# Kernel optimization log

Hardware: AMD Instinct MI355X
Metric: run time of the kernel (lower is better)

Reference implementation:

```python
import jax, jax.numpy as jnp
import numpy as np

D_MODEL = 1024
N_HEADS = 16
D_K = D_MODEL // N_HEADS


def setup_inputs() -> dict:
    key = jax.random.key(0)
    ks = jax.random.split(key, 12)
    B, S, D, H = 2, 2048, D_MODEL, N_HEADS
    s = 1.0 / np.sqrt(D)
    inp = {
        "x": jax.random.normal(ks[0], (B, S, D), jnp.float32),
        "Wq": jax.random.normal(ks[1], (D, D), jnp.float32) * s,
        "bq": jnp.zeros((D,), jnp.float32),
        "Wk": jax.random.normal(ks[2], (D, D), jnp.float32) * s,
        "bk": jnp.zeros((D,), jnp.float32),
        "Wv": jax.random.normal(ks[3], (D, D), jnp.float32) * s,
        "bv": jnp.zeros((D,), jnp.float32),
        "Wo": jax.random.normal(ks[4], (D, D), jnp.float32) * s,
        "bo": jnp.zeros((D,), jnp.float32),
        "Wp": jax.random.normal(ks[5], (D, H), jnp.float32) * s,
        "bp": jnp.zeros((H,), jnp.float32),
        "alpha": jax.random.normal(ks[6], (H,), jnp.float32) * 0.1,
    }
    return inp


def reference(x, Wq, bq, Wk, bk, Wv, bv, Wo, bo, Wp, bp, alpha):
    B, S, D = x.shape
    H, dk = N_HEADS, D_K
    scale = dk ** -0.5
    # projections -> (B, H, S, dk)
    Q = (x @ Wq + bq).reshape(B, S, H, dk).transpose(0, 2, 1, 3)
    K = (x @ Wk + bk).reshape(B, S, H, dk).transpose(0, 2, 1, 3)
    V = (x @ Wv + bv).reshape(B, S, H, dk).transpose(0, 2, 1, 3)
    scores = jnp.einsum("bhid,bhjd->bhij", Q, K) * scale  # (B,H,S,S)
    # phase derived from x: (B,S,H) -> (B,H,S)
    phase = (x @ Wp + bp).transpose(0, 2, 1)
    # coherence(i,j) = cos(phi_i - phi_j), per batch/head
    coherence = jnp.cos(phase[:, :, :, None] - phase[:, :, None, :])
    scores = scores + alpha[None, :, None, None] * coherence
    attn = jax.nn.softmax(scores, axis=-1)
    out = jnp.einsum("bhij,bhjd->bhid", attn, V)  # (B,H,S,dk)
    out = out.transpose(0, 2, 1, 3).reshape(B, S, D)
    return out @ Wo + bo
```

## Files before the change

kernel.cpp:

```cpp
#include <hip/hip_runtime.h>
#include <math.h>


#define S_LEN 2048
#define NHEADS 16

typedef __attribute__((ext_vector_type(8))) short short8;
typedef __attribute__((ext_vector_type(4))) float floatx4;
typedef __attribute__((ext_vector_type(2))) float float2v;

__device__ inline unsigned short f2bf(float f) {
    union { float f; unsigned int i; } v; v.f = f;
    unsigned int u = v.i;
    return (unsigned short)((u + 0x7fffu + ((u >> 16) & 1u)) >> 16);
}
__device__ inline unsigned int pack2_bf16(float hi, float lo) {
    union { float f; unsigned int u; } a, b; a.f = hi; b.f = lo;
    return __builtin_amdgcn_perm(a.u, b.u, 0x07060302u);
}
__device__ inline void async_copy16(const unsigned short* src, unsigned short* dst_lds) {
    __builtin_amdgcn_global_load_lds(
        (const __attribute__((address_space(1))) unsigned int*)(src),
        (__attribute__((address_space(3))) unsigned int*)(dst_lds), 16, 0, 0);
}
__device__ inline void async_copy4(const float* src, float* dst_lds) {
    __builtin_amdgcn_global_load_lds(
        (const __attribute__((address_space(1))) unsigned int*)(src),
        (__attribute__((address_space(3))) unsigned int*)(dst_lds), 4, 0, 0);
}

__global__ __launch_bounds__(256) void prep_kernel(
    const float* __restrict__ x, const float* __restrict__ Wp,
    const float* __restrict__ bp,
    const float* __restrict__ w0, const float* __restrict__ w1,
    const float* __restrict__ w2, const float* __restrict__ w3,
    unsigned short* __restrict__ d0, unsigned short* __restrict__ d1,
    unsigned short* __restrict__ d2, unsigned short* __restrict__ d3,
    float* __restrict__ cosP, float* __restrict__ sinP,
    unsigned short* __restrict__ xb) {
    __shared__ __align__(16) unsigned short shmem[64 * 72];
    int t = threadIdx.x;
    if (blockIdx.x < 4096) {
        float* fb = reinterpret_cast<float*>(shmem);
        float* xs = fb;
        float4* red4 = reinterpret_cast<float4*>(fb + 1024);
        int bid = blockIdx.x;
        int b = bid >> 11, s = bid & 2047;
        const float* xr = x + (size_t)bid * 1024;
        float4 xv = *reinterpret_cast<const float4*>(&xr[t * 4]);
        {
            uint2 o;
            o.x = (unsigned int)f2bf(xv.x) | ((unsigned int)f2bf(xv.y) << 16);
            o.y = (unsigned int)f2bf(xv.z) | ((unsigned int)f2bf(xv.w) << 16);
            *reinterpret_cast<uint2*>(&xb[(size_t)bid * 1024 + t * 4]) = o;
        }
        *reinterpret_cast<float4*>(&xs[t * 4]) = xv;
        __syncthreads();
        float f0 = 0.f, f1 = 0.f, f2 = 0.f, f3 = 0.f;
        int krow = t >> 2;
        const float4* wp4 = reinterpret_cast<const float4*>(Wp);
#pragma unroll
        for (int i = 0; i < 16; i++) {
            float4 wv = wp4[i * 256 + t];
            float xk = xs[i * 64 + krow];
            f0 += xk * wv.x; f1 += xk * wv.y; f2 += xk * wv.z; f3 += xk * wv.w;
        }
        red4[t] = make_float4(f0, f1, f2, f3);
        __syncthreads();
        if (t < 16) {
            int b2 = t >> 2, comp = t & 3;
            const float* rf = fb + 1024;
            float sum = bp[t];
#pragma unroll
            for (int j = 0; j < 64; j++) sum += rf[(4 * j + b2) * 4 + comp];
            float sv, cv;
            __sincosf(sum, &sv, &cv);
            size_t o = ((size_t)b * NHEADS + t) * S_LEN + s;
            cosP[o] = cv; sinP[o] = sv;
        }
    } else {
        unsigned short (*tile)[72] = reinterpret_cast<unsigned short (*)[72]>(shmem);
        int bid = blockIdx.x - 4096;
        int mat = bid >> 8;
        int tl  = bid & 255;
        int tr = tl >> 4, tc = tl & 15;
        const float* src    = (mat == 0) ? w0 : (mat == 1) ? w1 : (mat == 2) ? w2 : w3;
        unsigned short* dst = (mat == 0) ? d0 : (mat == 1) ? d1 : (mat == 2) ? d2 : d3;
        int col = t & 63, rbase = (t >> 6) * 16;
#pragma unroll
        for (int i = 0; i < 16; i++) {
            int row = rbase + i;
            tile[row][col] = f2bf(src[(size_t)(tr * 64 + row) * 1024 + tc * 64 + col]);
        }
        __syncthreads();
#pragma unroll
        for (int i = 0; i < 16; i++) {
            int row = rbase + i;
            dst[(size_t)(tc * 64 + row) * 1024 + tr * 64 + col] = tile[col][row];
        }
    }
}

template <int MT>
__global__ __launch_bounds__(256) void gemm_bt(
    const unsigned short* __restrict__ A, const unsigned short* __restrict__ BT,
    int N, int mode,
    const float* __restrict__ b0, const float* __restrict__ b1,
    const float* __restrict__ b2,
    unsigned short* __restrict__ o0, unsigned short* __restrict__ o1,
    unsigned short* __restrict__ o2, float* __restrict__ of) {
    __shared__ __align__(16) unsigned short As[2][MT * 32];
    __shared__ __align__(16) unsigned short Bs[2][128 * 32];
    const int K = 1024;
    const int MI = MT / 32;
    int t = threadIdx.x;
    int mBase = blockIdx.x * MT;
    int nBase = blockIdx.y * 128;
    int w = t >> 6, lane = t & 63, l15 = lane & 15, quad = lane >> 4;
    int wm = (w & 1) * (MT / 2), wn = (w >> 1) * 64;
    floatx4 acc[MI][4];
#pragma unroll
    for (int i = 0; i < MI; i++)
#pragma unroll
        for (int j = 0; j < 4; j++) acc[i][j] = (floatx4){0.f, 0.f, 0.f, 0.f};

    int arow = t >> 2, aseg = (t & 3) * 8;
#pragma unroll
    for (int i = 0; i < MT / 64; i++)
        async_copy16(&A[(size_t)(mBase + i * 64 + arow) * K + aseg],
                     &As[0][(i * 64 + arow) * 32 + aseg]);
#pragma unroll
    for (int i = 0; i < 2; i++)
        async_copy16(&BT[(size_t)(nBase + i * 64 + arow) * K + aseg],
                     &Bs[0][(i * 64 + arow) * 32 + aseg]);

    for (int k0 = 0; k0 < K; k0 += 32) {
        int cur = (k0 >> 5) & 1;
        __syncthreads();
        if (k0 + 32 < K) {
            int nb = cur ^ 1, kn = k0 + 32;
#pragma unroll
            for (int i = 0; i < MT / 64; i++)
                async_copy16(&A[(size_t)(mBase + i * 64 + arow) * K + kn + aseg],
                             &As[nb][(i * 64 + arow) * 32 + aseg]);
#pragma unroll
            for (int i = 0; i < 2; i++)
                async_copy16(&BT[(size_t)(nBase + i * 64 + arow) * K + kn + aseg],
                             &Bs[nb][(i * 64 + arow) * 32 + aseg]);
        }
        short8 af[MI], bfr[4];
#pragma unroll
        for (int mi = 0; mi < MI; mi++)
            af[mi] = *reinterpret_cast<const short8*>(&As[cur][(wm + mi * 16 + l15) * 32 + quad * 8]);
#pragma unroll
        for (int ni = 0; ni < 4; ni++)
            bfr[ni] = *reinterpret_cast<const short8*>(&Bs[cur][(wn + ni * 16 + l15) * 32 + quad * 8]);
        __builtin_amdgcn_s_setprio(1);
#pragma unroll
        for (int mi = 0; mi < MI; mi++)
#pragma unroll
            for (int ni = 0; ni < 4; ni++)
                acc[mi][ni] = __builtin_amdgcn_mfma_f32_16x16x32_bf16(af[mi], bfr[ni], acc[mi][ni], 0, 0, 0);
        __builtin_amdgcn_s_setprio(0);
    }

#pragma unroll
    for (int mi = 0; mi < MI; mi++) {
        int rowB = mBase + wm + mi * 16 + quad * 4;
#pragma unroll
        for (int ni = 0; ni < 4; ni++) {
            int col = nBase + wn + ni * 16 + l15;
            if (mode == 0) {
                float bias = b0[col];
#pragma unroll
                for (int r = 0; r < 4; r++) {
                    of[(size_t)(rowB + r) * N + col] = acc[mi][ni][r] + bias;
                }
            } else {
                int mat = col >> 10, nn = col & 1023;
                int h = nn >> 6, d = nn & 63;
                int b = rowB >> 11, sidx = rowB & 2047;
                if (mat == 2) {
                    float bv = b2[nn];
                    int jj = sidx & 63;
                    size_t rowOff = ((size_t)((b * NHEADS + h) * 64 + d)) * S_LEN +
                                    (sidx & ~63);
#pragma unroll
                    for (int r = 0; r < 4; r++) {
                        int j2 = jj + r;
                        int jt = j2 >> 4;
                        int u = (jt >> 1) * 32 + ((j2 & 15) >> 2) * 8 + (jt & 1) * 4 + (j2 & 3);
                        o2[rowOff + u] = f2bf(acc[mi][ni][r] + bv);
                    }
                } else {
                    const float* bias  = (mat == 0) ? b0 : b1;
                    unsigned short* op = (mat == 0) ? o0 : o1;
                    float bv = bias[nn];
                    float scl = (mat == 0) ? 0.18033688f : 1.0f;
#pragma unroll
                    for (int r = 0; r < 4; r++) {
                        float cv = (acc[mi][ni][r] + bv) * scl;
                        op[(((size_t)b * NHEADS + h) * S_LEN + (sidx + r)) * 64 + d] = f2bf(cv);
                    }
                }
            }
        }
    }
}

__global__ __launch_bounds__(1024) void attn_kernel(
    const unsigned short* __restrict__ Qg, const unsigned short* __restrict__ Kg,
    const unsigned short* __restrict__ VTg,
    const float* __restrict__ cosP, const float* __restrict__ sinP,
    const float* __restrict__ alpha, unsigned short* __restrict__ ctx) {
    __shared__ __align__(16) unsigned short KsB[4][64 * 64];
    __shared__ __align__(16) unsigned short VtB[4][64 * 64];
    __shared__ __align__(16) float csB[4][128];

    int x = blockIdx.x;
    int bh = (x & 7) * 4 + (x >> 6);
    int qt = (x >> 3) & 7;
    int t = threadIdx.x, w = t >> 6, lane = t & 63, l15 = lane & 15, quad = lane >> 4;
    int m0 = qt * 256 + w * 16;
    size_t base = (size_t)bh * (S_LEN * 64);
    size_t phBase = (size_t)bh * S_LEN;
    const float L2E = 1.44269504f;

    int th = t & 511;
    int sj = th >> 3, sg = th & 7;
    int srot = ((sg - (sj & 7)) & 7) * 8;
    bool stK = (t < 512);

    short8 qf[2];
#pragma unroll
    for (int c = 0; c < 2; c++)
        qf[c] = *reinterpret_cast<const short8*>(
            &Qg[base + (size_t)(m0 + l15) * 64 + c * 32 + quad * 8]);

    float alph = alpha[bh & 15] * L2E;
    float ci = alph * cosP[phBase + m0 + l15];
    float si = alph * sinP[phBase + m0 + l15];
    float2v ci2 = (float2v){ci, ci}, si2 = (float2v){si, si};

    {
#pragma unroll
        for (int t0 = 0; t0 < 2; t0++) {
            if (stK) async_copy16(&Kg[base + (size_t)(t0 * 64 + sj) * 64 + srot], &KsB[t0][th * 8]);
            else     async_copy16(&VTg[base + (size_t)sj * S_LEN + t0 * 64 + srot], &VtB[t0][th * 8]);
            if (w == 4)      async_copy4(&cosP[phBase + t0 * 64 + lane], &csB[t0][lane]);
            else if (w == 5) async_copy4(&sinP[phBase + t0 * 64 + lane], &csB[t0][64 + lane]);
        }
    }

    floatx4 oacc[4], lacc;
#pragma unroll
    for (int tt = 0; tt < 4; tt++) oacc[tt] = (floatx4){0.f, 0.f, 0.f, 0.f};
    lacc = (floatx4){0.f, 0.f, 0.f, 0.f};
    const short8 ones8 = {(short)0x3F80, (short)0x3F80, (short)0x3F80, (short)0x3F80,
                          (short)0x3F80, (short)0x3F80, (short)0x3F80, (short)0x3F80};

    int rot = l15 & 7;
    int cb0 = 16 * ((quad + rot) & 7);
    int cb1 = 16 * ((quad + 4 + rot) & 7);

    for (int kt = 0; kt < 32; kt++) {
        int p = kt & 3;
        if ((kt & 1) == 0) {
            __syncthreads();
#pragma unroll
            for (int d = 2; d <= 3; d++) {
                int kn = kt + d;
                if (kn < 32) {
                    int pn = kn & 3;
                    if (stK) async_copy16(&Kg[base + (size_t)(kn * 64 + sj) * 64 + srot], &KsB[pn][th * 8]);
                    else     async_copy16(&VTg[base + (size_t)sj * S_LEN + kn * 64 + srot], &VtB[pn][th * 8]);
                    if (w == 4)      async_copy4(&cosP[phBase + kn * 64 + lane], &csB[pn][lane]);
                    else if (w == 5) async_copy4(&sinP[phBase + kn * 64 + lane], &csB[pn][64 + lane]);
                }
            }
        }

        floatx4 st[4];
        __builtin_amdgcn_s_setprio(1);
#pragma unroll
        for (int jt = 0; jt < 4; jt++) {
            const char* kr = (const char*)&KsB[p][(jt * 16 + l15) * 64];
            short8 kf0 = *reinterpret_cast<const short8*>(kr + cb0);
            short8 kf1 = *reinterpret_cast<const short8*>(kr + cb1);
            floatx4 s = (floatx4){0.f, 0.f, 0.f, 0.f};
            s = __builtin_amdgcn_mfma_f32_16x16x32_bf16(kf0, qf[0], s, 0, 0, 0);
            s = __builtin_amdgcn_mfma_f32_16x16x32_bf16(kf1, qf[1], s, 0, 0, 0);
            st[jt] = s;
        }
        __builtin_amdgcn_s_setprio(0);

        union PW { unsigned int u[4]; short8 s8; };
        PW P0, P1;
#pragma unroll
        for (int jt = 0; jt < 4; jt++) {
            float4 cj4 = *reinterpret_cast<const float4*>(&csB[p][jt * 16 + quad * 4]);
            float4 sj4 = *reinterpret_cast<const float4*>(&csB[p][64 + jt * 16 + quad * 4]);
            float2v st01 = (float2v){st[jt][0], st[jt][1]};
            float2v st23 = (float2v){st[jt][2], st[jt][3]};
            float2v c01 = (float2v){cj4.x, cj4.y}, c23 = (float2v){cj4.z, cj4.w};
            float2v s01 = (float2v){sj4.x, sj4.y}, s23 = (float2v){sj4.z, sj4.w};
            float2v a01 = si2 * s01 + (ci2 * c01 + st01);
            float2v a23 = si2 * s23 + (ci2 * c23 + st23);
            unsigned int wA = pack2_bf16(__builtin_amdgcn_exp2f(a01.y),
                                         __builtin_amdgcn_exp2f(a01.x));
            unsigned int wB = pack2_bf16(__builtin_amdgcn_exp2f(a23.y),
                                         __builtin_amdgcn_exp2f(a23.x));
            if (jt == 0)      { P0.u[0] = wA; P0.u[1] = wB; }
            else if (jt == 1) { P0.u[2] = wA; P0.u[3] = wB; }
            else if (jt == 2) { P1.u[0] = wA; P1.u[1] = wB; }
            else              { P1.u[2] = wA; P1.u[3] = wB; }
        }

        __builtin_amdgcn_s_setprio(1);
#pragma unroll
        for (int c = 0; c < 2; c++) {
            short8 pf = c ? P1.s8 : P0.s8;
            int cb = c ? cb1 : cb0;
#pragma unroll
            for (int tt = 0; tt < 4; tt++) {
                const char* vr = (const char*)&VtB[p][(tt * 16 + l15) * 64];
                short8 vf = *reinterpret_cast<const short8*>(vr + cb);
                oacc[tt] = __builtin_amdgcn_mfma_f32_16x16x32_bf16(pf, vf, oacc[tt], 0, 0, 0);
            }
            lacc = __builtin_amdgcn_mfma_f32_16x16x32_bf16(pf, ones8, lacc, 0, 0, 0);
        }
        __builtin_amdgcn_s_setprio(0);
    }

    int b = bh >> 4, h = bh & 15;
    float inv[4];
#pragma unroll
    for (int r = 0; r < 4; r++) inv[r] = 1.0f / lacc[r];
#pragma unroll
    for (int tt = 0; tt < 4; tt++)
#pragma unroll
        for (int r = 0; r < 4; r++) {
            int srow = m0 + quad * 4 + r;
            ctx[((size_t)(b * S_LEN + srow)) * 1024 + h * 64 + tt * 16 + l15] =
                f2bf(oacc[tt][r] * inv[r]);
        }
}

extern "C" void kernel_launch(void* const* d_in, const int* in_sizes, int n_in,
                              void* d_out, int out_size, void* d_ws, size_t ws_size,
                              hipStream_t stream) {
    const float* x     = (const float*)d_in[0];
    const float* Wq    = (const float*)d_in[1];
    const float* bq    = (const float*)d_in[2];
    const float* Wk    = (const float*)d_in[3];
    const float* bk    = (const float*)d_in[4];
    const float* Wv    = (const float*)d_in[5];
    const float* bv    = (const float*)d_in[6];
    const float* Wo    = (const float*)d_in[7];
    const float* bo    = (const float*)d_in[8];
    const float* Wp    = (const float*)d_in[9];
    const float* bp    = (const float*)d_in[10];
    const float* alpha = (const float*)d_in[11];
    float* out = (float*)d_out;

    const size_t MB = 1048576;
    char* ws = (char*)d_ws;
    unsigned short* WT   = (unsigned short*)(ws);
    unsigned short* WoT  = (unsigned short*)(ws + 6 * MB);
    unsigned short* xb   = (unsigned short*)(ws + 8 * MB);
    unsigned short* ctx  = (unsigned short*)(ws + 8 * MB);
    unsigned short* Qw   = (unsigned short*)(ws + 16 * MB);
    unsigned short* Kw   = (unsigned short*)(ws + 24 * MB);
    unsigned short* VTg  = (unsigned short*)(ws + 32 * MB);
    float* cosP          = (float*)(ws + 40 * MB);
    float* sinP          = (float*)(ws + 40 * MB + 262144);

    prep_kernel<<<dim3(5120), dim3(256), 0, stream>>>(
        x, Wp, bp, Wq, Wk, Wv, Wo,
        WT, WT + 1048576, WT + 2097152, WoT, cosP, sinP, xb);
    gemm_bt<128><<<dim3(32, 24), dim3(256), 0, stream>>>(
        xb, WT, 3072, 1, bq, bk, bv, Qw, Kw, VTg, (float*)nullptr);
    attn_kernel<<<dim3(256), dim3(1024), 0, stream>>>(
        Qw, Kw, VTg, cosP, sinP, alpha, ctx);
    gemm_bt<64><<<dim3(64, 8), dim3(256), 0, stream>>>(
        ctx, WoT, 1024, 0, bo, bo, bo,
        (unsigned short*)nullptr, (unsigned short*)nullptr,
        (unsigned short*)nullptr, out);
}
```

Measured before the change: 203.5 us.

## Process 32 query rows per wave in attention to reuse K/V fragments

The attention kernel now runs 8 waves of 512 threads instead of 16 waves, and each wave handles two 16-row query sub-tiles. Each K and V fragment read from LDS, and each cos/sin value, now feeds two MFMAs, which halves LDS traffic per unit of work. Every thread now issues both the K and the V async copy. The cost is higher register pressure from doubled accumulators and fewer waves per CU to hide latency.

```diff
diff --git a/kernel.cpp b/kernel.cpp
--- a/kernel.cpp
+++ b/kernel.cpp
@@ -208,7 +208,7 @@
     }
 }
 
-__global__ __launch_bounds__(1024) void attn_kernel(
+__global__ __launch_bounds__(512) void attn_kernel(
     const unsigned short* __restrict__ Qg, const unsigned short* __restrict__ Kg,
     const unsigned short* __restrict__ VTg,
     const float* __restrict__ cosP, const float* __restrict__ sinP,
@@ -221,41 +221,48 @@
     int bh = (x & 7) * 4 + (x >> 6);
     int qt = (x >> 3) & 7;
     int t = threadIdx.x, w = t >> 6, lane = t & 63, l15 = lane & 15, quad = lane >> 4;
-    int m0 = qt * 256 + w * 16;
+    int m0 = qt * 256 + w * 32;
     size_t base = (size_t)bh * (S_LEN * 64);
     size_t phBase = (size_t)bh * S_LEN;
     const float L2E = 1.44269504f;
 
-    int th = t & 511;
-    int sj = th >> 3, sg = th & 7;
+    int sj = t >> 3, sg = t & 7;
     int srot = ((sg - (sj & 7)) & 7) * 8;
-    bool stK = (t < 512);
-
-    short8 qf[2];
-#pragma unroll
-    for (int c = 0; c < 2; c++)
-        qf[c] = *reinterpret_cast<const short8*>(
-            &Qg[base + (size_t)(m0 + l15) * 64 + c * 32 + quad * 8]);
+
+    short8 qf[2][2];
+#pragma unroll
+    for (int rh = 0; rh < 2; rh++)
+#pragma unroll
+        for (int c = 0; c < 2; c++)
+            qf[rh][c] = *reinterpret_cast<const short8*>(
+                &Qg[base + (size_t)(m0 + rh * 16 + l15) * 64 + c * 32 + quad * 8]);
 
     float alph = alpha[bh & 15] * L2E;
-    float ci = alph * cosP[phBase + m0 + l15];
-    float si = alph * sinP[phBase + m0 + l15];
-    float2v ci2 = (float2v){ci, ci}, si2 = (float2v){si, si};
+    float2v ci2[2], si2[2];
+#pragma unroll
+    for (int rh = 0; rh < 2; rh++) {
+        float ci = alph * cosP[phBase + m0 + rh * 16 + l15];
+        float si = alph * sinP[phBase + m0 + rh * 16 + l15];
+        ci2[rh] = (float2v){ci, ci}; si2[rh] = (float2v){si, si};
+    }
 
     {
 #pragma unroll
         for (int t0 = 0; t0 < 2; t0++) {
-            if (stK) async_copy16(&Kg[base + (size_t)(t0 * 64 + sj) * 64 + srot], &KsB[t0][th * 8]);
-            else     async_copy16(&VTg[base + (size_t)sj * S_LEN + t0 * 64 + srot], &VtB[t0][th * 8]);
+            async_copy16(&Kg[base + (size_t)(t0 * 64 + sj) * 64 + srot], &KsB[t0][t * 8]);
+            async_copy16(&VTg[base + (size_t)sj * S_LEN + t0 * 64 + srot], &VtB[t0][t * 8]);
             if (w == 4)      async_copy4(&cosP[phBase + t0 * 64 + lane], &csB[t0][lane]);
             else if (w == 5) async_copy4(&sinP[phBase + t0 * 64 + lane], &csB[t0][64 + lane]);
         }
     }
 
-    floatx4 oacc[4], lacc;
-#pragma unroll
-    for (int tt = 0; tt < 4; tt++) oacc[tt] = (floatx4){0.f, 0.f, 0.f, 0.f};
-    lacc = (floatx4){0.f, 0.f, 0.f, 0.f};
+    floatx4 oacc[2][4], lacc[2];
+#pragma unroll
+    for (int rh = 0; rh < 2; rh++) {
+#pragma unroll
+        for (int tt = 0; tt < 4; tt++) oacc[rh][tt] = (floatx4){0.f, 0.f, 0.f, 0.f};
+        lacc[rh] = (floatx4){0.f, 0.f, 0.f, 0.f};
+    }
     const short8 ones8 = {(short)0x3F80, (short)0x3F80, (short)0x3F80, (short)0x3F80,
                           (short)0x3F80, (short)0x3F80, (short)0x3F80, (short)0x3F80};
 
@@ -272,78 +279,97 @@
                 int kn = kt + d;
                 if (kn < 32) {
                     int pn = kn & 3;
-                    if (stK) async_copy16(&Kg[base + (size_t)(kn * 64 + sj) * 64 + srot], &KsB[pn][th * 8]);
-                    else     async_copy16(&VTg[base + (size_t)sj * S_LEN + kn * 64 + srot], &VtB[pn][th * 8]);
+                    async_copy16(&Kg[base + (size_t)(kn * 64 + sj) * 64 + srot], &KsB[pn][t * 8]);
+                    async_copy16(&VTg[base + (size_t)sj * S_LEN + kn * 64 + srot], &VtB[pn][t * 8]);
                     if (w == 4)      async_copy4(&cosP[phBase + kn * 64 + lane], &csB[pn][lane]);
                     else if (w == 5) async_copy4(&sinP[phBase + kn * 64 + lane], &csB[pn][64 + lane]);
                 }
             }
         }
 
-        floatx4 st[4];
+        floatx4 st[2][4];
         __builtin_amdgcn_s_setprio(1);
 #pragma unroll
         for (int jt = 0; jt < 4; jt++) {
             const char* kr = (const char*)&KsB[p][(jt * 16 + l15) * 64];
             short8 kf0 = *reinterpret_cast<const short8*>(kr + cb0);
             short8 kf1 = *reinterpret_cast<const short8*>(kr + cb1);
-            floatx4 s = (floatx4){0.f, 0.f, 0.f, 0.f};
-            s = __builtin_amdgcn_mfma_f32_16x16x32_bf16(kf0, qf[0], s, 0, 0, 0);
-            s = __builtin_amdgcn_mfma_f32_16x16x32_bf16(kf1, qf[1], s, 0, 0, 0);
-            st[jt] = s;
+#pragma unroll
+            for (int rh = 0; rh < 2; rh++) {
+                floatx4 s = (floatx4){0.f, 0.f, 0.f, 0.f};
+                s = __builtin_amdgcn_mfma_f32_16x16x32_bf16(kf0, qf[rh][0], s, 0, 0, 0);
+                s = __builtin_amdgcn_mfma_f32_16x16x32_bf16(kf1, qf[rh][1], s, 0, 0, 0);
+                st[rh][jt] = s;
+            }
         }
         __builtin_amdgcn_s_setprio(0);
 
+        float4 cj4[4], sj4[4];
+#pragma unroll
+        for (int jt = 0; jt < 4; jt++) {
+            cj4[jt] = *reinterpret_cast<const float4*>(&csB[p][jt * 16 + quad * 4]);
+            sj4[jt] = *reinterpret_cast<const float4*>(&csB[p][64 + jt * 16 + quad * 4]);
+        }
+
         union PW { unsigned int u[4]; short8 s8; };
-        PW P0, P1;
-#pragma unroll
-        for (int jt = 0; jt < 4; jt++) {
-            float4 cj4 = *reinterpret_cast<const float4*>(&csB[p][jt * 16 + quad * 4]);
-            float4 sj4 = *reinterpret_cast<const float4*>(&csB[p][64 + jt * 16 + quad * 4]);
-            float2v st01 = (float2v){st[jt][0], st[jt][1]};
-            float2v st23 = (float2v){st[jt][2], st[jt][3]};
-            float2v c01 = (float2v){cj4.x, cj4.y}, c23 = (float2v){cj4.z, cj4.w};
-            float2v s01 = (float2v){sj4.x, sj4.y}, s23 = (float2v){sj4.z, sj4.w};
-            float2v a01 = si2 * s01 + (ci2 * c01 + st01);
-            float2v a23 = si2 * s23 + (ci2 * c23 + st23);
-            unsigned int wA = pack2_bf16(__builtin_amdgcn_exp2f(a01.y),
-                                         __builtin_amdgcn_exp2f(a01.x));
-            unsigned int wB = pack2_bf16(__builtin_amdgcn_exp2f(a23.y),
-                                         __builtin_amdgcn_exp2f(a23.x));
-            if (jt == 0)      { P0.u[0] = wA; P0.u[1] = wB; }
-            else if (jt == 1) { P0.u[2] = wA; P0.u[3] = wB; }
-            else if (jt == 2) { P1.u[0] = wA; P1.u[1] = wB; }
-            else              { P1.u[2] = wA; P1.u[3] = wB; }
+        PW P0[2], P1[2];
+#pragma unroll
+        for (int rh = 0; rh < 2; rh++) {
+#pragma unroll
+            for (int jt = 0; jt < 4; jt++) {
+                float2v st01 = (float2v){st[rh][jt][0], st[rh][jt][1]};
+                float2v st23 = (float2v){st[rh][jt][2], st[rh][jt][3]};
+                float2v c01 = (float2v){cj4[jt].x, cj4[jt].y};
+                float2v c23 = (float2v){cj4[jt].z, cj4[jt].w};
+                float2v s01 = (float2v){sj4[jt].x, sj4[jt].y};
+                float2v s23 = (float2v){sj4[jt].z, sj4[jt].w};
+                float2v a01 = si2[rh] * s01 + (ci2[rh] * c01 + st01);
+                float2v a23 = si2[rh] * s23 + (ci2[rh] * c23 + st23);
+                unsigned int wA = pack2_bf16(__builtin_amdgcn_exp2f(a01.y),
+                                             __builtin_amdgcn_exp2f(a01.x));
+                unsigned int wB = pack2_bf16(__builtin_amdgcn_exp2f(a23.y),
+                                             __builtin_amdgcn_exp2f(a23.x));
+                if (jt == 0)      { P0[rh].u[0] = wA; P0[rh].u[1] = wB; }
+                else if (jt == 1) { P0[rh].u[2] = wA; P0[rh].u[3] = wB; }
+                else if (jt == 2) { P1[rh].u[0] = wA; P1[rh].u[1] = wB; }
+                else              { P1[rh].u[2] = wA; P1[rh].u[3] = wB; }
+            }
         }
 
         __builtin_amdgcn_s_setprio(1);
 #pragma unroll
         for (int c = 0; c < 2; c++) {
-            short8 pf = c ? P1.s8 : P0.s8;
             int cb = c ? cb1 : cb0;
+            short8 pfa = c ? P1[0].s8 : P0[0].s8;
+            short8 pfb = c ? P1[1].s8 : P0[1].s8;
 #pragma unroll
             for (int tt = 0; tt < 4; tt++) {
                 const char* vr = (const char*)&VtB[p][(tt * 16 + l15) * 64];
                 short8 vf = *reinterpret_cast<const short8*>(vr + cb);
-                oacc[tt] = __builtin_amdgcn_mfma_f32_16x16x32_bf16(pf, vf, oacc[tt], 0, 0, 0);
-            }
-            lacc = __builtin_amdgcn_mfma_f32_16x16x32_bf16(pf, ones8, lacc, 0, 0, 0);
+                oacc[0][tt] = __builtin_amdgcn_mfma_f32_16x16x32_bf16(pfa, vf, oacc[0][tt], 0, 0, 0);
+                oacc[1][tt] = __builtin_amdgcn_mfma_f32_16x16x32_bf16(pfb, vf, oacc[1][tt], 0, 0, 0);
+            }
+            lacc[0] = __builtin_amdgcn_mfma_f32_16x16x32_bf16(pfa, ones8, lacc[0], 0, 0, 0);
+            lacc[1] = __builtin_amdgcn_mfma_f32_16x16x32_bf16(pfb, ones8, lacc[1], 0, 0, 0);
         }
         __builtin_amdgcn_s_setprio(0);
     }
 
     int b = bh >> 4, h = bh & 15;
-    float inv[4];
-#pragma unroll
-    for (int r = 0; r < 4; r++) inv[r] = 1.0f / lacc[r];
-#pragma unroll
-    for (int tt = 0; tt < 4; tt++)
-#pragma unroll
-        for (int r = 0; r < 4; r++) {
-            int srow = m0 + quad * 4 + r;
-            ctx[((size_t)(b * S_LEN + srow)) * 1024 + h * 64 + tt * 16 + l15] =
-                f2bf(oacc[tt][r] * inv[r]);
-        }
+#pragma unroll
+    for (int rh = 0; rh < 2; rh++) {
+        float inv[4];
+#pragma unroll
+        for (int r = 0; r < 4; r++) inv[r] = 1.0f / lacc[rh][r];
+#pragma unroll
+        for (int tt = 0; tt < 4; tt++)
+#pragma unroll
+            for (int r = 0; r < 4; r++) {
+                int srow = m0 + rh * 16 + quad * 4 + r;
+                ctx[((size_t)(b * S_LEN + srow)) * 1024 + h * 64 + tt * 16 + l15] =
+                    f2bf(oacc[rh][tt][r] * inv[r]);
+            }
+    }
 }
 
 extern "C" void kernel_launch(void* const* d_in, const int* in_sizes, int n_in,
@@ -380,7 +406,7 @@
         WT, WT + 1048576, WT + 2097152, WoT, cosP, sinP, xb);
     gemm_bt<128><<<dim3(32, 24), dim3(256), 0, stream>>>(
         xb, WT, 3072, 1, bq, bk, bv, Qw, Kw, VTg, (float*)nullptr);
-    attn_kernel<<<dim3(256), dim3(1024), 0, stream>>>(
+    attn_kernel<<<dim3(256), dim3(512), 0, stream>>>(
         Qw, Kw, VTg, cosP, sinP, alpha, ctx);
     gemm_bt<64><<<dim3(64, 8), dim3(256), 0, stream>>>(
         ctx, WoT, 1024, 0, bo, bo, bo,
```

After: 204.5 us. About the same (+0.5%).
